# Performance work log

Hardware: AMD Instinct MI355X
Metric: run time of the kernel (lower is better)

Reference implementation:

```python
import jax, jax.numpy as jnp
import numpy as np

jax.config.update("jax_enable_x64", True)  # needed for faithful float64 bit reinterpretation

VOCAB = 50257
HIDDEN = 1024
MAX_POS = 4096
TYPE_VOCAB = 2
NUM_FEATS = 94
PROJ_INTER = 256
NUM_TOKEN_ID = 5
LN_EPS = 1e-12


def _layer_norm(x, g, b, eps=LN_EPS):
    mu = jnp.mean(x, axis=-1, keepdims=True)
    var = jnp.var(x, axis=-1, keepdims=True)
    return (x - mu) * jax.lax.rsqrt(var + eps) * g + b


def _numeric_features(values, formats):
    # values: [B,S] float32 (torch casts to float64 internally), formats: [B,S] int
    v = values.astype(jnp.float64)
    # float64_binary_repr (64 bits). Torch: (int64_view & (1<<i)) > 0; bit 63 mask
    # overflows to INT64_MIN so (x & mask) > 0 is always False -> replicate exactly.
    bits = jax.lax.bitcast_convert_type(v, jnp.int64)
    masks = jnp.left_shift(jnp.int64(1), jnp.arange(64, dtype=jnp.int64))
    binary = ((bits[..., None] & masks) > 0).astype(jnp.float32)  # [B,S,64]
    av = jnp.abs(v)
    fl = jnp.floor(av)
    units = jnp.clip(fl % 10.0, 0, 9).astype(jnp.int32)
    oh_units = jax.nn.one_hot(units, 10, dtype=jnp.float32)       # [B,S,10]
    tens = jnp.clip((fl // 10.0) % 10.0, 0, 9).astype(jnp.int32)
    oh_tens = jax.nn.one_hot(tens, 10, dtype=jnp.float32)         # [B,S,10]
    log_v = jnp.log(av + 1e-6).astype(jnp.float32)
    sign = jnp.sign(v).astype(jnp.float32)
    expo = jnp.where(av > 1e-6, jnp.floor(jnp.log10(jnp.maximum(av, 1e-300))), 0.0).astype(jnp.float32)
    is_int = (av == fl).astype(jnp.float32)
    is_pos = (v > 0).astype(jnp.float32)
    is_zero = (v == 0.0).astype(jnp.float32)
    is_neg = (v < 0).astype(jnp.float32)
    pos_int = (v == jnp.floor(v)) & (v > 0)
    l2 = jnp.log2(jnp.maximum(v, 1.0))
    is_pow2 = (pos_int & (l2 == jnp.floor(l2))).astype(jnp.float32)
    fmt_int = (formats == 0).astype(jnp.float32)
    fmt_float = (formats == 1).astype(jnp.float32)
    scalars = jnp.stack([log_v, sign, expo, is_int, is_pos, is_zero, is_neg, is_pow2, fmt_int, fmt_float], axis=-1)
    return jnp.concatenate([binary, oh_units, oh_tens, scalars], axis=-1)  # [B,S,94]


def setup_inputs() -> dict:
    key = jax.random.key(0)
    ks = jax.random.split(key, 12)
    B, S = 8, 2048
    input_ids = jax.random.randint(ks[0], (B, S), 0, VOCAB, dtype=jnp.int64)
    numeric_values = jax.random.normal(ks[1], (B, S), dtype=jnp.float32) * 100.0
    numeric_formats = jax.random.randint(ks[2], (B, S), 0, 2, dtype=jnp.int64)
    s = 0.02
    W_word = (jax.random.normal(ks[3], (VOCAB, HIDDEN), dtype=jnp.float32) * s).at[0].set(0.0)  # padding_idx=0
    W_pos = jax.random.normal(ks[4], (MAX_POS, HIDDEN), dtype=jnp.float32) * s
    W_type = jax.random.normal(ks[5], (TYPE_VOCAB, HIDDEN), dtype=jnp.float32) * s
    ln_g = jnp.ones((HIDDEN,), jnp.float32)
    ln_b = jnp.zeros((HIDDEN,), jnp.float32)
    p_w1 = jax.random.normal(ks[6], (NUM_FEATS, PROJ_INTER), dtype=jnp.float32) * s
    p_b1 = jnp.zeros((PROJ_INTER,), jnp.float32)
    p_w2 = jax.random.normal(ks[7], (PROJ_INTER, HIDDEN), dtype=jnp.float32) * s
    p_b2 = jnp.zeros((HIDDEN,), jnp.float32)
    pln_g = jnp.ones((HIDDEN,), jnp.float32)
    pln_b = jnp.zeros((HIDDEN,), jnp.float32)
    return dict(input_ids=input_ids, numeric_values=numeric_values, numeric_formats=numeric_formats,
                W_word=W_word, W_pos=W_pos, W_type=W_type, ln_g=ln_g, ln_b=ln_b,
                p_w1=p_w1, p_b1=p_b1, p_w2=p_w2, p_b2=p_b2, pln_g=pln_g, pln_b=pln_b)


def reference(input_ids, numeric_values, numeric_formats, W_word, W_pos, W_type,
              ln_g, ln_b, p_w1, p_b1, p_w2, p_b2, pln_g, pln_b):
    B, S = input_ids.shape
    # text embeddings: word + position + token_type (token_type_ids default = 0)
    text = W_word[input_ids] + W_pos[jnp.arange(S)][None, :, :] + W_type[0][None, None, :]
    text = text.astype(jnp.float32)
    # active numeric positions: [NUM] token AND non-NaN value
    active = (input_ids == NUM_TOKEN_ID) & ~jnp.isnan(numeric_values)  # [B,S]
    safe_vals = jnp.where(active, numeric_values, 1.0)
    feats = _numeric_features(safe_vals, numeric_formats)  # [B,S,94] float32
    # numeric projection MLP: Linear -> GELU -> Linear -> LayerNorm
    h = jax.nn.gelu(feats @ p_w1 + p_b1, approximate=False)
    num_emb = _layer_norm(h @ p_w2 + p_b2, pln_g, pln_b)
    num_emb = jnp.where(active[..., None], num_emb, 0.0)  # scatter into zeros
    # fusion_type == 'add', then final LayerNorm (dropout p=0 -> identity)
    out = _layer_norm(text + num_emb, ln_g, ln_b)
    return out
```

## Files before the change

### kernel.cpp

```cpp
#include <hip/hip_runtime.h>
#include <math.h>

#define HIDDEN 1024
#define SEQ 2048
#define NF 94
#define PI 256
#define NUM_TOKEN 5

typedef float vfloat4 __attribute__((ext_vector_type(4)));

__device__ __forceinline__ float gelu_exact(float a) {
    return 0.5f * a * (1.0f + erff(a * 0.70710678118654752f));
}

__global__ __launch_bounds__(256)
void blackhole_emb_kernel(const int* __restrict__ ids,
                          const float* __restrict__ vals,
                          const int* __restrict__ fmts,
                          const float* __restrict__ Ww,
                          const float* __restrict__ Wp,
                          const float* __restrict__ Wt,
                          const float* __restrict__ lng,
                          const float* __restrict__ lnb,
                          const float* __restrict__ w1,
                          const float* __restrict__ b1,
                          const float* __restrict__ w2,
                          const float* __restrict__ b2,
                          const float* __restrict__ plng,
                          const float* __restrict__ plnb,
                          float* __restrict__ out,
                          int tokens)
{
    const int lane  = threadIdx.x & 63;
    const int wv    = threadIdx.x >> 6;
    const int token = blockIdx.x * 4 + wv;
    if (token >= tokens) return;
    const int s = token & (SEQ - 1);

    const int   id     = ids[token];
    const float vraw   = vals[token];
    const bool  active = (id == NUM_TOKEN) && !isnan(vraw);

    const float* wrow = Ww + (size_t)id * HIDDEN;
    const float* prow = Wp + (size_t)s  * HIDDEN;
    const int    col0 = lane * 4;

    float x[4][4];
    #pragma unroll
    for (int j = 0; j < 4; ++j) {
        const int off = j * 256 + col0;
        const float4 aw = *(const float4*)(wrow + off);
        const float4 ap = *(const float4*)(prow + off);
        const float4 at = *(const float4*)(Wt   + off);
        x[j][0] = aw.x + ap.x + at.x;
        x[j][1] = aw.y + ap.y + at.y;
        x[j][2] = aw.z + ap.z + at.z;
        x[j][3] = aw.w + ap.w + at.w;
    }

    if (active) {
        const double    v    = (double)vraw;
        const double    av   = fabs(v);
        const long long bits = __double_as_longlong(v);
        const double    fl   = floor(av);
        const int       fmt  = fmts[token];

        float f0 = (lane < 63 && ((bits >> lane) & 1LL)) ? 1.0f : 0.0f;
        float f1 = 0.0f;
        if (lane < 10) {
            const int units = (int)fmin(fmax(fmod(fl, 10.0), 0.0), 9.0);
            f1 = (lane == units) ? 1.0f : 0.0f;
        } else if (lane < 20) {
            const int tens = (int)fmin(fmax(fmod(floor(fl / 10.0), 10.0), 0.0), 9.0);
            f1 = (lane - 10 == tens) ? 1.0f : 0.0f;
        } else if (lane < 30) {
            switch (lane - 20) {
                case 0: f1 = (float)log(av + 1e-6); break;
                case 1: f1 = (v > 0.0) ? 1.0f : ((v < 0.0) ? -1.0f : 0.0f); break;
                case 2: f1 = (av > 1e-6) ? (float)floor(log10(fmax(av, 1e-300))) : 0.0f; break;
                case 3: f1 = (av == fl) ? 1.0f : 0.0f; break;
                case 4: f1 = (v > 0.0) ? 1.0f : 0.0f; break;
                case 5: f1 = (v == 0.0) ? 1.0f : 0.0f; break;
                case 6: f1 = (v < 0.0) ? 1.0f : 0.0f; break;
                case 7: {
                    const bool   pos_int = (v == floor(v)) && (v > 0.0);
                    const double l2      = log2(fmax(v, 1.0));
                    f1 = (pos_int && (l2 == floor(l2))) ? 1.0f : 0.0f;
                    break;
                }
                case 8: f1 = (fmt == 0) ? 1.0f : 0.0f; break;
                case 9: f1 = (fmt == 1) ? 1.0f : 0.0f; break;
            }
        }

        float acc[4] = { b1[lane], b1[lane + 64], b1[lane + 128], b1[lane + 192] };
        for (int k = 0; k < 64; ++k) {
            const float  fk  = __shfl(f0, k, 64);
            const float* col = w1 + k * PI;
            acc[0] = fmaf(fk, col[lane],       acc[0]);
            acc[1] = fmaf(fk, col[lane + 64],  acc[1]);
            acc[2] = fmaf(fk, col[lane + 128], acc[2]);
            acc[3] = fmaf(fk, col[lane + 192], acc[3]);
        }
        for (int k = 0; k < NF - 64; ++k) {
            const float  fk  = __shfl(f1, k, 64);
            const float* col = w1 + (64 + k) * PI;
            acc[0] = fmaf(fk, col[lane],       acc[0]);
            acc[1] = fmaf(fk, col[lane + 64],  acc[1]);
            acc[2] = fmaf(fk, col[lane + 128], acc[2]);
            acc[3] = fmaf(fk, col[lane + 192], acc[3]);
        }
        float h[4];
        #pragma unroll
        for (int i = 0; i < 4; ++i) h[i] = gelu_exact(acc[i]);

        float n[4][4];
        #pragma unroll
        for (int j = 0; j < 4; ++j) {
            const float4 bb = *(const float4*)(b2 + j * 256 + col0);
            n[j][0] = bb.x; n[j][1] = bb.y; n[j][2] = bb.z; n[j][3] = bb.w;
        }
        #pragma unroll
        for (int i = 0; i < 4; ++i) {
            for (int kk = 0; kk < 64; ++kk) {
                const float  hk  = __shfl(h[i], kk, 64);
                const float* row = w2 + (size_t)(i * 64 + kk) * HIDDEN;
                #pragma unroll
                for (int j = 0; j < 4; ++j) {
                    const float4 w = *(const float4*)(row + j * 256 + col0);
                    n[j][0] = fmaf(hk, w.x, n[j][0]);
                    n[j][1] = fmaf(hk, w.y, n[j][1]);
                    n[j][2] = fmaf(hk, w.z, n[j][2]);
                    n[j][3] = fmaf(hk, w.w, n[j][3]);
                }
            }
        }

        float sm = 0.0f, sq = 0.0f;
        #pragma unroll
        for (int j = 0; j < 4; ++j)
            #pragma unroll
            for (int c = 0; c < 4; ++c) { sm += n[j][c]; sq += n[j][c] * n[j][c]; }
        #pragma unroll
        for (int off = 32; off > 0; off >>= 1) {
            sm += __shfl_xor(sm, off, 64);
            sq += __shfl_xor(sq, off, 64);
        }
        const float mu   = sm * (1.0f / HIDDEN);
        const float var  = sq * (1.0f / HIDDEN) - mu * mu;
        const float rstd = rsqrtf(var + 1e-12f);
        #pragma unroll
        for (int j = 0; j < 4; ++j) {
            const float4 g4 = *(const float4*)(plng + j * 256 + col0);
            const float4 b4 = *(const float4*)(plnb + j * 256 + col0);
            x[j][0] += (n[j][0] - mu) * rstd * g4.x + b4.x;
            x[j][1] += (n[j][1] - mu) * rstd * g4.y + b4.y;
            x[j][2] += (n[j][2] - mu) * rstd * g4.z + b4.z;
            x[j][3] += (n[j][3] - mu) * rstd * g4.w + b4.w;
        }
    }

    float sm = 0.0f, sq = 0.0f;
    #pragma unroll
    for (int j = 0; j < 4; ++j)
        #pragma unroll
        for (int c = 0; c < 4; ++c) { sm += x[j][c]; sq += x[j][c] * x[j][c]; }
    #pragma unroll
    for (int off = 32; off > 0; off >>= 1) {
        sm += __shfl_xor(sm, off, 64);
        sq += __shfl_xor(sq, off, 64);
    }
    const float mu   = sm * (1.0f / HIDDEN);
    const float var  = sq * (1.0f / HIDDEN) - mu * mu;
    const float rstd = rsqrtf(var + 1e-12f);

    float* orow = out + (size_t)token * HIDDEN;
    #pragma unroll
    for (int j = 0; j < 4; ++j) {
        const int off = j * 256 + col0;
        const float4 g4 = *(const float4*)(lng + off);
        const float4 b4 = *(const float4*)(lnb + off);
        vfloat4 o;
        o.x = (x[j][0] - mu) * rstd * g4.x + b4.x;
        o.y = (x[j][1] - mu) * rstd * g4.y + b4.y;
        o.z = (x[j][2] - mu) * rstd * g4.z + b4.z;
        o.w = (x[j][3] - mu) * rstd * g4.w + b4.w;
        __builtin_nontemporal_store(o, (vfloat4*)(orow + off));
    }
}

extern "C" void kernel_launch(void* const* d_in, const int* in_sizes, int n_in,
                              void* d_out, int out_size, void* d_ws, size_t ws_size,
                              hipStream_t stream) {
    const int*   ids  = (const int*)d_in[0];
    const float* vals = (const float*)d_in[1];
    const int*   fmts = (const int*)d_in[2];
    const float* Ww   = (const float*)d_in[3];
    const float* Wp   = (const float*)d_in[4];
    const float* Wt   = (const float*)d_in[5];
    const float* lng  = (const float*)d_in[6];
    const float* lnb  = (const float*)d_in[7];
    const float* w1   = (const float*)d_in[8];
    const float* b1   = (const float*)d_in[9];
    const float* w2   = (const float*)d_in[10];
    const float* b2   = (const float*)d_in[11];
    const float* plng = (const float*)d_in[12];
    const float* plnb = (const float*)d_in[13];
    float* out = (float*)d_out;

    const int tokens = in_sizes[0];
    const int blocks = (tokens + 3) / 4;
    blackhole_emb_kernel<<<blocks, 256, 0, stream>>>(
        ids, vals, fmts, Ww, Wp, Wt, lng, lnb, w1, b1, w2, b2, plng, plnb, out, tokens);
}
```

Before: 304.5 us.

## Split into text-LN kernel and compacted numeric-token fixup kernel

Splits the fused kernel in two. The first kernel writes LayerNorm(text embedding) for every token. The second kernel ballots the active [NUM] tokens within each group of 64 and recomputes and overwrites only those rows with the numeric MLP added. The aim is to stop divergent, heavy MLP work from stalling waves in the bandwidth-bound main pass. In exchange it adds a second launch, rewrites active rows, and serializes up to 64 active tokens per wave.

```diff
diff --git a/kernel.cpp b/kernel.cpp
--- a/kernel.cpp
+++ b/kernel.cpp
@@ -14,36 +14,25 @@
 }
 
 __global__ __launch_bounds__(256)
-void blackhole_emb_kernel(const int* __restrict__ ids,
-                          const float* __restrict__ vals,
-                          const int* __restrict__ fmts,
-                          const float* __restrict__ Ww,
-                          const float* __restrict__ Wp,
-                          const float* __restrict__ Wt,
-                          const float* __restrict__ lng,
-                          const float* __restrict__ lnb,
-                          const float* __restrict__ w1,
-                          const float* __restrict__ b1,
-                          const float* __restrict__ w2,
-                          const float* __restrict__ b2,
-                          const float* __restrict__ plng,
-                          const float* __restrict__ plnb,
-                          float* __restrict__ out,
-                          int tokens)
+void text_ln_kernel(const int* __restrict__ ids,
+                    const float* __restrict__ Ww,
+                    const float* __restrict__ Wp,
+                    const float* __restrict__ Wt,
+                    const float* __restrict__ lng,
+                    const float* __restrict__ lnb,
+                    float* __restrict__ out,
+                    int tokens)
 {
     const int lane  = threadIdx.x & 63;
     const int wv    = threadIdx.x >> 6;
     const int token = blockIdx.x * 4 + wv;
     if (token >= tokens) return;
-    const int s = token & (SEQ - 1);
-
-    const int   id     = ids[token];
-    const float vraw   = vals[token];
-    const bool  active = (id == NUM_TOKEN) && !isnan(vraw);
+    const int s    = token & (SEQ - 1);
+    const int id   = ids[token];
+    const int col0 = lane * 4;
 
     const float* wrow = Ww + (size_t)id * HIDDEN;
     const float* prow = Wp + (size_t)s  * HIDDEN;
-    const int    col0 = lane * 4;
 
     float x[4][4];
     #pragma unroll
@@ -58,12 +47,92 @@
         x[j][3] = aw.w + ap.w + at.w;
     }
 
-    if (active) {
+    float sm = 0.0f, sq = 0.0f;
+    #pragma unroll
+    for (int j = 0; j < 4; ++j)
+        #pragma unroll
+        for (int c = 0; c < 4; ++c) { sm += x[j][c]; sq += x[j][c] * x[j][c]; }
+    #pragma unroll
+    for (int off = 32; off > 0; off >>= 1) {
+        sm += __shfl_xor(sm, off, 64);
+        sq += __shfl_xor(sq, off, 64);
+    }
+    const float mu   = sm * (1.0f / HIDDEN);
+    const float var  = sq * (1.0f / HIDDEN) - mu * mu;
+    const float rstd = rsqrtf(var + 1e-12f);
+
+    float* orow = out + (size_t)token * HIDDEN;
+    #pragma unroll
+    for (int j = 0; j < 4; ++j) {
+        const int off = j * 256 + col0;
+        const float4 g4 = *(const float4*)(lng + off);
+        const float4 b4 = *(const float4*)(lnb + off);
+        vfloat4 o;
+        o.x = (x[j][0] - mu) * rstd * g4.x + b4.x;
+        o.y = (x[j][1] - mu) * rstd * g4.y + b4.y;
+        o.z = (x[j][2] - mu) * rstd * g4.z + b4.z;
+        o.w = (x[j][3] - mu) * rstd * g4.w + b4.w;
+        __builtin_nontemporal_store(o, (vfloat4*)(orow + off));
+    }
+}
+
+__global__ __launch_bounds__(256)
+void numeric_fix_kernel(const int* __restrict__ ids,
+                        const float* __restrict__ vals,
+                        const int* __restrict__ fmts,
+                        const float* __restrict__ Ww,
+                        const float* __restrict__ Wp,
+                        const float* __restrict__ Wt,
+                        const float* __restrict__ lng,
+                        const float* __restrict__ lnb,
+                        const float* __restrict__ w1,
+                        const float* __restrict__ b1,
+                        const float* __restrict__ w2,
+                        const float* __restrict__ b2,
+                        const float* __restrict__ plng,
+                        const float* __restrict__ plnb,
+                        float* __restrict__ out,
+                        int tokens)
+{
+    const int lane = threadIdx.x & 63;
+    const int wv   = threadIdx.x >> 6;
+    const int base = (blockIdx.x * 4 + wv) * 64;
+    if (base >= tokens) return;
+
+    const int   myid  = ids[base + lane];
+    const float myval = vals[base + lane];
+    unsigned long long mask = __ballot((myid == NUM_TOKEN) && !isnan(myval));
+
+    const int col0 = lane * 4;
+
+    while (mask) {
+        const int t = __ffsll((unsigned long long)mask) - 1;
+        mask &= mask - 1;
+        const int token = base + t;
+        const int s     = token & (SEQ - 1);
+
+        const float vraw = __shfl(myval, t, 64);
+        const int   fmt  = fmts[token];
+
         const double    v    = (double)vraw;
         const double    av   = fabs(v);
         const long long bits = __double_as_longlong(v);
         const double    fl   = floor(av);
-        const int       fmt  = fmts[token];
+
+        const float* wrow = Ww + (size_t)NUM_TOKEN * HIDDEN;
+        const float* prow = Wp + (size_t)s * HIDDEN;
+        float x[4][4];
+        #pragma unroll
+        for (int j = 0; j < 4; ++j) {
+            const int off = j * 256 + col0;
+            const float4 aw = *(const float4*)(wrow + off);
+            const float4 ap = *(const float4*)(prow + off);
+            const float4 at = *(const float4*)(Wt   + off);
+            x[j][0] = aw.x + ap.x + at.x;
+            x[j][1] = aw.y + ap.y + at.y;
+            x[j][2] = aw.z + ap.z + at.z;
+            x[j][3] = aw.w + ap.w + at.w;
+        }
 
         float f0 = (lane < 63 && ((bits >> lane) & 1LL)) ? 1.0f : 0.0f;
         float f1 = 0.0f;
@@ -146,46 +215,48 @@
             sm += __shfl_xor(sm, off, 64);
             sq += __shfl_xor(sq, off, 64);
         }
+        {
+            const float mu   = sm * (1.0f / HIDDEN);
+            const float var  = sq * (1.0f / HIDDEN) - mu * mu;
+            const float rstd = rsqrtf(var + 1e-12f);
+            #pragma unroll
+            for (int j = 0; j < 4; ++j) {
+                const float4 g4 = *(const float4*)(plng + j * 256 + col0);
+                const float4 b4 = *(const float4*)(plnb + j * 256 + col0);
+                x[j][0] += (n[j][0] - mu) * rstd * g4.x + b4.x;
+                x[j][1] += (n[j][1] - mu) * rstd * g4.y + b4.y;
+                x[j][2] += (n[j][2] - mu) * rstd * g4.z + b4.z;
+                x[j][3] += (n[j][3] - mu) * rstd * g4.w + b4.w;
+            }
+        }
+
+        sm = 0.0f; sq = 0.0f;
+        #pragma unroll
+        for (int j = 0; j < 4; ++j)
+            #pragma unroll
+            for (int c = 0; c < 4; ++c) { sm += x[j][c]; sq += x[j][c] * x[j][c]; }
+        #pragma unroll
+        for (int off = 32; off > 0; off >>= 1) {
+            sm += __shfl_xor(sm, off, 64);
+            sq += __shfl_xor(sq, off, 64);
+        }
         const float mu   = sm * (1.0f / HIDDEN);
         const float var  = sq * (1.0f / HIDDEN) - mu * mu;
         const float rstd = rsqrtf(var + 1e-12f);
+
+        float* orow = out + (size_t)token * HIDDEN;
         #pragma unroll
         for (int j = 0; j < 4; ++j) {
-            const float4 g4 = *(const float4*)(plng + j * 256 + col0);
-            const float4 b4 = *(const float4*)(plnb + j * 256 + col0);
-            x[j][0] += (n[j][0] - mu) * rstd * g4.x + b4.x;
-            x[j][1] += (n[j][1] - mu) * rstd * g4.y + b4.y;
-            x[j][2] += (n[j][2] - mu) * rstd * g4.z + b4.z;
-            x[j][3] += (n[j][3] - mu) * rstd * g4.w + b4.w;
-        }
-    }
-
-    float sm = 0.0f, sq = 0.0f;
-    #pragma unroll
-    for (int j = 0; j < 4; ++j)
-        #pragma unroll
-        for (int c = 0; c < 4; ++c) { sm += x[j][c]; sq += x[j][c] * x[j][c]; }
-    #pragma unroll
-    for (int off = 32; off > 0; off >>= 1) {
-        sm += __shfl_xor(sm, off, 64);
-        sq += __shfl_xor(sq, off, 64);
-    }
-    const float mu   = sm * (1.0f / HIDDEN);
-    const float var  = sq * (1.0f / HIDDEN) - mu * mu;
-    const float rstd = rsqrtf(var + 1e-12f);
-
-    float* orow = out + (size_t)token * HIDDEN;
-    #pragma unroll
-    for (int j = 0; j < 4; ++j) {
-        const int off = j * 256 + col0;
-        const float4 g4 = *(const float4*)(lng + off);
-        const float4 b4 = *(const float4*)(lnb + off);
-        vfloat4 o;
-        o.x = (x[j][0] - mu) * rstd * g4.x + b4.x;
-        o.y = (x[j][1] - mu) * rstd * g4.y + b4.y;
-        o.z = (x[j][2] - mu) * rstd * g4.z + b4.z;
-        o.w = (x[j][3] - mu) * rstd * g4.w + b4.w;
-        __builtin_nontemporal_store(o, (vfloat4*)(orow + off));
+            const int off = j * 256 + col0;
+            const float4 g4 = *(const float4*)(lng + off);
+            const float4 b4 = *(const float4*)(lnb + off);
+            float4 o;
+            o.x = (x[j][0] - mu) * rstd * g4.x + b4.x;
+            o.y = (x[j][1] - mu) * rstd * g4.y + b4.y;
+            o.z = (x[j][2] - mu) * rstd * g4.z + b4.z;
+            o.w = (x[j][3] - mu) * rstd * g4.w + b4.w;
+            *(float4*)(orow + off) = o;
+        }
     }
 }
 
@@ -209,7 +280,11 @@
     float* out = (float*)d_out;
 
     const int tokens = in_sizes[0];
-    const int blocks = (tokens + 3) / 4;
-    blackhole_emb_kernel<<<blocks, 256, 0, stream>>>(
+
+    text_ln_kernel<<<(tokens + 3) / 4, 256, 0, stream>>>(
+        ids, Ww, Wp, Wt, lng, lnb, out, tokens);
+
+    const int blocksB = (tokens + 255) / 256;
+    numeric_fix_kernel<<<blocksB, 256, 0, stream>>>(
         ids, vals, fmts, Ww, Wp, Wt, lng, lnb, w1, b1, w2, b2, plng, plnb, out, tokens);
 }
```

After: 309.1 us. Within noise of the previous version (+1.5%).
